# Performance work log

Hardware: AMD Instinct MI355X
Metric: run time of the kernel (lower is better)

The kernel has to match this reference:

```python
import jax, jax.numpy as jnp
import numpy as np

N = 4_000_000          # total nodes in batch
NUM_GRAPHS = 1024      # number of graphs (batch ids in [0, 1024))
D_OUT = 3              # pred/target feature dim
D_X = 8                # node feature dim (cols 3:5 are force components)
MIN_SCALE = 0.1


def setup_inputs() -> dict:
    key = jax.random.key(0)
    k1, k2, k3, k4 = jax.random.split(key, 4)
    pred = jax.random.normal(k1, (N, D_OUT), dtype=jnp.float32)
    target = jax.random.normal(k2, (N, D_OUT), dtype=jnp.float32)
    # PyG-style batch vector: sorted graph ids per node
    batch = jnp.sort(jax.random.randint(k3, (N,), 0, NUM_GRAPHS, dtype=jnp.int32))
    x = jax.random.normal(k4, (N, D_X), dtype=jnp.float32)
    return {"pred": pred, "target": target, "batch": batch, "x": x}


def reference(pred, target, batch, x):
    # per-node sum of |pred - target| over feature dim  -> [N]
    abs_sum = jnp.sum(jnp.abs(pred - target), axis=1)
    ones = jnp.ones_like(abs_sum)
    seg_sum = jax.ops.segment_sum(abs_sum, batch, num_segments=NUM_GRAPHS)   # [G]
    counts = jax.ops.segment_sum(ones, batch, num_segments=NUM_GRAPHS)       # [G]
    # graph-wise mean over ALL elements (nodes * features); guard empty graphs
    graph_mae = seg_sum / (jnp.maximum(counts, 1.0) * pred.shape[1])
    # original loop calls compute_total_force on the FULL x every iteration,
    # so the scale is global; .item() detaches it from the graph.
    total_force = jnp.sum(jnp.linalg.norm(x[:, 3:5], axis=1))
    scale = jax.lax.stop_gradient(jnp.maximum(total_force, MIN_SCALE))
    return jnp.mean(graph_mae * scale) * 100.0
```

## Files before the change

kernel.cpp:

```cpp
#include <hip/hip_runtime.h>

#define NUM_GRAPHS 1024
#define BLOCK 256
#define GROUPS_PER_THREAD 2
#define NODES_PER_BLOCK (BLOCK * GROUPS_PER_THREAD * 4)

__global__ __launch_bounds__(BLOCK, 8) void mae_seg_kernel(
    const float* __restrict__ pred,
    const float* __restrict__ target,
    const int*   __restrict__ batch,
    const float* __restrict__ x,
    float* __restrict__ ws_sum,
    float* __restrict__ ws_cnt,
    float* __restrict__ ws_force,
    int n)
{
    __shared__ float ls[NUM_GRAPHS];
    __shared__ float lc[NUM_GRAPHS];
    __shared__ float lf[BLOCK / 64];

    const int tid      = threadIdx.x;
    const int node0    = blockIdx.x * NODES_PER_BLOCK;
    const int node_end = min(node0 + NODES_PER_BLOCK, n);
    const bool full    = (node0 + NODES_PER_BLOCK) <= n;

    const int b_lo = batch[node0];
    const int b_hi = batch[node_end - 1];
    for (int i = b_lo + tid; i <= b_hi; i += BLOCK) { ls[i] = 0.f; lc[i] = 0.f; }
    __syncthreads();

    const float4* p4 = (const float4*)pred;
    const float4* t4 = (const float4*)target;
    const int4*   b4 = (const int4*)batch;

    int   cur_id  = -1;
    float cur_sum = 0.f;
    float cur_cnt = 0.f;

    const int group_base = blockIdx.x * (BLOCK * GROUPS_PER_THREAD);
    if (full) {
#pragma unroll
        for (int v = 0; v < GROUPS_PER_THREAD; ++v) {
            const int g = group_base + v * BLOCK + tid;
            float4 pa = p4[g * 3 + 0], pb = p4[g * 3 + 1], pc = p4[g * 3 + 2];
            float4 ta = t4[g * 3 + 0], tb = t4[g * 3 + 1], tc = t4[g * 3 + 2];
            int4   bb = b4[g];
            float asum[4];
            asum[0] = fabsf(pa.x - ta.x) + fabsf(pa.y - ta.y) + fabsf(pa.z - ta.z);
            asum[1] = fabsf(pa.w - ta.w) + fabsf(pb.x - tb.x) + fabsf(pb.y - tb.y);
            asum[2] = fabsf(pb.z - tb.z) + fabsf(pb.w - tb.w) + fabsf(pc.x - tc.x);
            asum[3] = fabsf(pc.y - tc.y) + fabsf(pc.z - tc.z) + fabsf(pc.w - tc.w);
            int bid[4] = {bb.x, bb.y, bb.z, bb.w};
#pragma unroll
            for (int r = 0; r < 4; ++r) {
                if (bid[r] != cur_id) {
                    if (cur_id >= 0) {
                        atomicAdd(&ls[cur_id], cur_sum);
                        atomicAdd(&lc[cur_id], cur_cnt);
                    }
                    cur_id = bid[r]; cur_sum = 0.f; cur_cnt = 0.f;
                }
                cur_sum += asum[r];
                cur_cnt += 1.f;
            }
        }
    } else {
        for (int v = 0; v < GROUPS_PER_THREAD; ++v) {
            const int node = (group_base + v * BLOCK + tid) * 4;
            for (int r = 0; r < 4; ++r) {
                const int nd = node + r;
                if (nd >= n) break;
                float a = fabsf(pred[nd * 3 + 0] - target[nd * 3 + 0])
                        + fabsf(pred[nd * 3 + 1] - target[nd * 3 + 1])
                        + fabsf(pred[nd * 3 + 2] - target[nd * 3 + 2]);
                int b = batch[nd];
                if (b != cur_id) {
                    if (cur_id >= 0) {
                        atomicAdd(&ls[cur_id], cur_sum);
                        atomicAdd(&lc[cur_id], cur_cnt);
                    }
                    cur_id = b; cur_sum = 0.f; cur_cnt = 0.f;
                }
                cur_sum += a;
                cur_cnt += 1.f;
            }
        }
    }

    {
        const int id0 = __shfl(cur_id, 0, 64);
        if (__all(cur_id == id0)) {
            float s = cur_sum, c = cur_cnt;
#pragma unroll
            for (int off = 32; off > 0; off >>= 1) {
                s += __shfl_xor(s, off, 64);
                c += __shfl_xor(c, off, 64);
            }
            if ((tid & 63) == 0 && id0 >= 0) {
                atomicAdd(&ls[id0], s);
                atomicAdd(&lc[id0], c);
            }
        } else if (cur_id >= 0) {
            atomicAdd(&ls[cur_id], cur_sum);
            atomicAdd(&lc[cur_id], cur_cnt);
        }
    }

    const float4* x4 = (const float4*)x;
    const int xbase = blockIdx.x * (NODES_PER_BLOCK * 2);
    float fsum = 0.f;
    if (full) {
#pragma unroll
        for (int half = 0; half < 2; ++half) {
            const int i0 = xbase + half * 8 * BLOCK;
            float4 xv[8];
#pragma unroll
            for (int v = 0; v < 8; ++v) xv[v] = x4[i0 + v * BLOCK + tid];
#pragma unroll
            for (int v = 0; v < 8; ++v) {
                const float val = (tid & 1) ? xv[v].x : xv[v].w;
                const float oth = __shfl_xor(val, 1, 64);
                fsum += sqrtf(val * val + oth * oth);
            }
        }
    } else {
        const int nx4 = n * 2;
#pragma unroll
        for (int v = 0; v < 16; ++v) {
            const int idx = xbase + v * BLOCK + tid;
            float val = 0.f;
            if (idx < nx4) {
                float4 xv = x4[idx];
                val = (tid & 1) ? xv.x : xv.w;
            }
            const float oth = __shfl_xor(val, 1, 64);
            fsum += sqrtf(val * val + oth * oth);
        }
    }
    fsum *= 0.5f;
#pragma unroll
    for (int off = 32; off > 0; off >>= 1) fsum += __shfl_down(fsum, off, 64);
    if ((tid & 63) == 0) lf[tid >> 6] = fsum;
    __syncthreads();
    if (tid == 0) {
        atomicAdd(ws_force, lf[0] + lf[1] + lf[2] + lf[3]);
    }

    for (int i = b_lo + tid; i <= b_hi; i += BLOCK) {
        float c = lc[i];
        if (c != 0.f) {
            atomicAdd(&ws_sum[i], ls[i]);
            atomicAdd(&ws_cnt[i], c);
        }
    }
}

__global__ __launch_bounds__(NUM_GRAPHS) void finalize_kernel(
    const float* __restrict__ ws_sum,
    const float* __restrict__ ws_cnt,
    const float* __restrict__ ws_force,
    float* __restrict__ out)
{
    __shared__ float red[NUM_GRAPHS];
    const int t = threadIdx.x;
    red[t] = ws_sum[t] / (fmaxf(ws_cnt[t], 1.0f) * 3.0f);
    __syncthreads();
    for (int s = NUM_GRAPHS / 2; s > 0; s >>= 1) {
        if (t < s) red[t] += red[t + s];
        __syncthreads();
    }
    if (t == 0) {
        const float scale = fmaxf(ws_force[0], 0.1f);
        out[0] = (red[0] / (float)NUM_GRAPHS) * scale * 100.0f;
    }
}

extern "C" void kernel_launch(void* const* d_in, const int* in_sizes, int n_in,
                              void* d_out, int out_size, void* d_ws, size_t ws_size,
                              hipStream_t stream) {
    const float* pred   = (const float*)d_in[0];
    const float* target = (const float*)d_in[1];
    const int*   batch  = (const int*)d_in[2];
    const float* x      = (const float*)d_in[3];
    float* out = (float*)d_out;

    const int n = in_sizes[2];

    float* ws_sum   = (float*)d_ws;
    float* ws_cnt   = ws_sum + NUM_GRAPHS;
    float* ws_force = ws_cnt + NUM_GRAPHS;

    hipMemsetAsync(d_ws, 0, (2 * NUM_GRAPHS + 1) * sizeof(float), stream);

    const int blocks = (n + NODES_PER_BLOCK - 1) / NODES_PER_BLOCK;
    mae_seg_kernel<<<blocks, BLOCK, 0, stream>>>(pred, target, batch, x,
                                                 ws_sum, ws_cnt, ws_force, n);
    finalize_kernel<<<1, NUM_GRAPHS, 0, stream>>>(ws_sum, ws_cnt, ws_force, out);
}
```

Measured before the change: 58.52 us.

## Double-buffer tile loads with interleaved force reduction and larger per-block chunks

Measured after the change: 51.27 us (median of 3 runs). 12.4% less time.

```diff
diff --git a/kernel.cpp b/kernel.cpp
--- a/kernel.cpp
+++ b/kernel.cpp
@@ -2,10 +2,11 @@
 
 #define NUM_GRAPHS 1024
 #define BLOCK 256
-#define GROUPS_PER_THREAD 2
-#define NODES_PER_BLOCK (BLOCK * GROUPS_PER_THREAD * 4)
-
-__global__ __launch_bounds__(BLOCK, 8) void mae_seg_kernel(
+#define TILE_NODES 1024
+#define TILES_PER_BLOCK 4
+#define CHUNK (TILE_NODES * TILES_PER_BLOCK)
+
+__global__ __launch_bounds__(BLOCK, 2) void mae_seg_kernel(
     const float* __restrict__ pred,
     const float* __restrict__ target,
     const int*   __restrict__ batch,
@@ -20,9 +21,9 @@
     __shared__ float lf[BLOCK / 64];
 
     const int tid      = threadIdx.x;
-    const int node0    = blockIdx.x * NODES_PER_BLOCK;
-    const int node_end = min(node0 + NODES_PER_BLOCK, n);
-    const bool full    = (node0 + NODES_PER_BLOCK) <= n;
+    const int node0    = blockIdx.x * CHUNK;
+    if (node0 >= n) return;
+    const int node_end = min(node0 + CHUNK, n);
 
     const int b_lo = batch[node0];
     const int b_hi = batch[node_end - 1];
@@ -32,41 +33,82 @@
     const float4* p4 = (const float4*)pred;
     const float4* t4 = (const float4*)target;
     const int4*   b4 = (const int4*)batch;
+    const float4* x4 = (const float4*)x;
 
     int   cur_id  = -1;
     float cur_sum = 0.f;
     float cur_cnt = 0.f;
-
-    const int group_base = blockIdx.x * (BLOCK * GROUPS_PER_THREAD);
-    if (full) {
-#pragma unroll
-        for (int v = 0; v < GROUPS_PER_THREAD; ++v) {
-            const int g = group_base + v * BLOCK + tid;
-            float4 pa = p4[g * 3 + 0], pb = p4[g * 3 + 1], pc = p4[g * 3 + 2];
-            float4 ta = t4[g * 3 + 0], tb = t4[g * 3 + 1], tc = t4[g * 3 + 2];
-            int4   bb = b4[g];
-            float asum[4];
-            asum[0] = fabsf(pa.x - ta.x) + fabsf(pa.y - ta.y) + fabsf(pa.z - ta.z);
-            asum[1] = fabsf(pa.w - ta.w) + fabsf(pb.x - tb.x) + fabsf(pb.y - tb.y);
-            asum[2] = fabsf(pb.z - tb.z) + fabsf(pb.w - tb.w) + fabsf(pc.x - tc.x);
-            asum[3] = fabsf(pc.y - tc.y) + fabsf(pc.z - tc.z) + fabsf(pc.w - tc.w);
-            int bid[4] = {bb.x, bb.y, bb.z, bb.w};
-#pragma unroll
-            for (int r = 0; r < 4; ++r) {
-                if (bid[r] != cur_id) {
-                    if (cur_id >= 0) {
-                        atomicAdd(&ls[cur_id], cur_sum);
-                        atomicAdd(&lc[cur_id], cur_cnt);
-                    }
-                    cur_id = bid[r]; cur_sum = 0.f; cur_cnt = 0.f;
-                }
-                cur_sum += asum[r];
-                cur_cnt += 1.f;
-            }
-        }
-    } else {
-        for (int v = 0; v < GROUPS_PER_THREAD; ++v) {
-            const int node = (group_base + v * BLOCK + tid) * 4;
+    float fsum    = 0.f;
+
+    int ft = (node_end - node0) / TILE_NODES;
+
+    float4 PA[3], TA[3], XA[8]; int4 BA;
+    float4 PB[3], TB[3], XB[8]; int4 BB;
+
+#define LOAD_TILE(t, P, T, B, X)                                          \
+    {                                                                     \
+        const int g0 = (node0 + (t) * TILE_NODES) / 4 + tid;              \
+        const int xb = (node0 + (t) * TILE_NODES) * 2;                    \
+        P[0] = p4[g0 * 3 + 0]; P[1] = p4[g0 * 3 + 1]; P[2] = p4[g0 * 3 + 2]; \
+        T[0] = t4[g0 * 3 + 0]; T[1] = t4[g0 * 3 + 1]; T[2] = t4[g0 * 3 + 2]; \
+        B    = b4[g0];                                                    \
+        X[0] = x4[xb + 0 * BLOCK + tid]; X[1] = x4[xb + 1 * BLOCK + tid]; \
+        X[2] = x4[xb + 2 * BLOCK + tid]; X[3] = x4[xb + 3 * BLOCK + tid]; \
+        X[4] = x4[xb + 4 * BLOCK + tid]; X[5] = x4[xb + 5 * BLOCK + tid]; \
+        X[6] = x4[xb + 6 * BLOCK + tid]; X[7] = x4[xb + 7 * BLOCK + tid]; \
+    }
+
+#define CONSUME_TILE(P, T, B, X)                                          \
+    {                                                                     \
+        float4 pa = P[0], pb = P[1], pc = P[2];                           \
+        float4 ta = T[0], tb = T[1], tc = T[2];                           \
+        float asum[4];                                                    \
+        asum[0] = fabsf(pa.x - ta.x) + fabsf(pa.y - ta.y) + fabsf(pa.z - ta.z); \
+        asum[1] = fabsf(pa.w - ta.w) + fabsf(pb.x - tb.x) + fabsf(pb.y - tb.y); \
+        asum[2] = fabsf(pb.z - tb.z) + fabsf(pb.w - tb.w) + fabsf(pc.x - tc.x); \
+        asum[3] = fabsf(pc.y - tc.y) + fabsf(pc.z - tc.z) + fabsf(pc.w - tc.w); \
+        int bid[4] = {B.x, B.y, B.z, B.w};                                \
+        if (bid[0] == cur_id && bid[3] == cur_id) {                       \
+            cur_sum += asum[0] + asum[1] + asum[2] + asum[3];             \
+            cur_cnt += 4.f;                                               \
+        } else {                                                          \
+            _Pragma("unroll")                                             \
+            for (int r = 0; r < 4; ++r) {                                 \
+                if (bid[r] != cur_id) {                                   \
+                    if (cur_id >= 0) {                                    \
+                        atomicAdd(&ls[cur_id], cur_sum);                  \
+                        atomicAdd(&lc[cur_id], cur_cnt);                  \
+                    }                                                     \
+                    cur_id = bid[r]; cur_sum = 0.f; cur_cnt = 0.f;        \
+                }                                                         \
+                cur_sum += asum[r];                                       \
+                cur_cnt += 1.f;                                           \
+            }                                                             \
+        }                                                                 \
+        _Pragma("unroll")                                                 \
+        for (int v = 0; v < 8; ++v) {                                     \
+            const float val = (tid & 1) ? X[v].x : X[v].w;                \
+            const float oth = __shfl_xor(val, 1, 64);                     \
+            fsum += sqrtf(val * val + oth * oth);                         \
+        }                                                                 \
+    }
+
+    if (ft >= 1) LOAD_TILE(0, PA, TA, BA, XA);
+    if (ft >= 2) LOAD_TILE(1, PB, TB, BB, XB);
+    if (ft >= 1) CONSUME_TILE(PA, TA, BA, XA);
+    if (ft >= 3) LOAD_TILE(2, PA, TA, BA, XA);
+    if (ft >= 2) CONSUME_TILE(PB, TB, BB, XB);
+    if (ft >= 4) LOAD_TILE(3, PB, TB, BB, XB);
+    if (ft >= 3) CONSUME_TILE(PA, TA, BA, XA);
+    if (ft >= 4) CONSUME_TILE(PB, TB, BB, XB);
+
+#undef LOAD_TILE
+#undef CONSUME_TILE
+
+    {
+        const int tnode0 = node0 + ft * TILE_NODES;
+        if (tnode0 < node_end) {
+            const int node = tnode0 + tid * 4;
             for (int r = 0; r < 4; ++r) {
                 const int nd = node + r;
                 if (nd >= n) break;
@@ -84,6 +126,19 @@
                 cur_sum += a;
                 cur_cnt += 1.f;
             }
+            const int xb  = tnode0 * 2;
+            const int nx4 = n * 2;
+#pragma unroll
+            for (int v = 0; v < 8; ++v) {
+                const int idx = xb + v * BLOCK + tid;
+                float val = 0.f;
+                if (idx < nx4) {
+                    float4 xv = x4[idx];
+                    val = (tid & 1) ? xv.x : xv.w;
+                }
+                const float oth = __shfl_xor(val, 1, 64);
+                fsum += sqrtf(val * val + oth * oth);
+            }
         }
     }
 
@@ -106,37 +161,6 @@
         }
     }
 
-    const float4* x4 = (const float4*)x;
-    const int xbase = blockIdx.x * (NODES_PER_BLOCK * 2);
-    float fsum = 0.f;
-    if (full) {
-#pragma unroll
-        for (int half = 0; half < 2; ++half) {
-            const int i0 = xbase + half * 8 * BLOCK;
-            float4 xv[8];
-#pragma unroll
-            for (int v = 0; v < 8; ++v) xv[v] = x4[i0 + v * BLOCK + tid];
-#pragma unroll
-            for (int v = 0; v < 8; ++v) {
-                const float val = (tid & 1) ? xv[v].x : xv[v].w;
-                const float oth = __shfl_xor(val, 1, 64);
-                fsum += sqrtf(val * val + oth * oth);
-            }
-        }
-    } else {
-        const int nx4 = n * 2;
-#pragma unroll
-        for (int v = 0; v < 16; ++v) {
-            const int idx = xbase + v * BLOCK + tid;
-            float val = 0.f;
-            if (idx < nx4) {
-                float4 xv = x4[idx];
-                val = (tid & 1) ? xv.x : xv.w;
-            }
-            const float oth = __shfl_xor(val, 1, 64);
-            fsum += sqrtf(val * val + oth * oth);
-        }
-    }
     fsum *= 0.5f;
 #pragma unroll
     for (int off = 32; off > 0; off >>= 1) fsum += __shfl_down(fsum, off, 64);
@@ -192,7 +216,7 @@
 
     hipMemsetAsync(d_ws, 0, (2 * NUM_GRAPHS + 1) * sizeof(float), stream);
 
-    const int blocks = (n + NODES_PER_BLOCK - 1) / NODES_PER_BLOCK;
+    const int blocks = (n + CHUNK - 1) / CHUNK;
     mae_seg_kernel<<<blocks, BLOCK, 0, stream>>>(pred, target, batch, x,
                                                  ws_sum, ws_cnt, ws_force, n);
     finalize_kernel<<<1, NUM_GRAPHS, 0, stream>>>(ws_sum, ws_cnt, ws_force, out);
```
